# Optimization experiments

Measured on AMD Instinct MI355X. Metric: run time of the kernel, lower is better.

The kernel has to match this reference:

```python
import jax, jax.numpy as jnp
import numpy as np

CH = 64          # channels
OC = 64          # out_channels
B, H, W = 8, 128, 128
NCA_C = CH + OC  # 128, NCA state channels
K = 3            # kernel_size
DILS = (1, 2, 4, 8)
HID = 64         # NCA update hidden
EPS = 1e-5


def setup_inputs() -> dict:
    key = jax.random.key(0)
    ks = jax.random.split(key, 16)
    def n(k, shape, s=0.02):
        return jax.random.normal(k, shape, jnp.float32) * s
    return {
        "x": jax.random.normal(ks[0], (B, H, W, CH), jnp.float32),
        "c": jax.random.normal(ks[1], (B, OC), jnp.float32),
        # Attention params
        "Wq": n(ks[2], (CH, OC)), "bq": jnp.zeros((OC,), jnp.float32),
        "Wk": n(ks[3], (OC, OC)), "bk": jnp.zeros((OC,), jnp.float32),
        "Wv": n(ks[4], (OC, OC)), "bv": jnp.zeros((OC,), jnp.float32),
        "Wo": n(ks[5], (OC, OC)), "bo": jnp.zeros((OC,), jnp.float32),
        "ln_g": jnp.ones((OC,), jnp.float32), "ln_b": jnp.zeros((OC,), jnp.float32),
        # NCA depthwise perception kernels, one per dilation: [4, NCA_C, 1, K, K]
        "pk": n(ks[6], (len(DILS), NCA_C, 1, K, K), 0.1),
        # NCA update MLP
        "W1": n(ks[7], ((1 + len(DILS)) * NCA_C, HID)), "b1": jnp.zeros((HID,), jnp.float32),
        "W2": n(ks[8], (HID, CH)), "b2": jnp.zeros((CH,), jnp.float32),
    }


def _layernorm(z, g, b):
    m = jnp.mean(z, axis=-1, keepdims=True)
    v = jnp.var(z, axis=-1, keepdims=True)
    return (z - m) / jnp.sqrt(v + EPS) * g + b


def _forward(x, c, Wq, bq, Wk, bk, Wv, bv, Wo, bo, ln_g, ln_b, pk, W1, b1, W2, b2):
    b_, h_, w_, _ = x.shape
    # ---- Attention(x, c): single-key softmax pooling over H*W ----
    q = x.reshape(b_, h_ * w_, CH) @ Wq + bq              # [B, HW, OC]
    k = c @ Wk + bk                                        # [B, OC]
    v = c @ Wv + bv                                        # [B, OC]
    scores = jnp.einsum('bno,bo->bn', q, k) * (OC ** -0.5)  # [B, HW]
    attn = jax.nn.softmax(scores, axis=1)                  # softmax over spatial dim
    attended = jnp.einsum('bn,bo->bo', attn, v)            # weighted pool (weights sum to 1)
    a = _layernorm(attended @ Wo + bo + c, ln_g, ln_b)     # out_proj + residual + LN
    c2 = c + a                                             # outer residual in NCAAttention

    # ---- concat broadcast context -> NCA state [B,H,W,NCA_C] ----
    c_exp = jnp.broadcast_to(c2[:, None, None, :], (b_, h_, w_, OC))
    xc = jnp.concatenate([x, c_exp], axis=-1)

    # ---- NCA perception: depthwise dilated convs (SAME padding) ----
    xp = jnp.transpose(xc, (0, 3, 1, 2))                   # NCHW
    feats = [xc]
    for i, d in enumerate(DILS):
        pad = d * (K // 2)
        p = jax.lax.conv_general_dilated(
            xp, pk[i], window_strides=(1, 1),
            padding=[(pad, pad), (pad, pad)], rhs_dilation=(d, d),
            dimension_numbers=('NCHW', 'OIHW', 'NCHW'),
            feature_group_count=NCA_C)
        feats.append(jnp.transpose(p, (0, 2, 3, 1)))
    upd_in = jnp.concatenate(feats, axis=-1)               # [B,H,W,5*NCA_C]

    # ---- NCA update MLP: Linear -> (Dropout=id) -> GELU -> Linear ----
    hidden = jax.nn.gelu(upd_in @ W1 + b1, approximate=False)
    y = hidden @ W2 + b2                                   # [B,H,W,CH]
    # NCA.out_channels (64) != NCA.channels (128) -> no residual add
    return y, c2


def reference(x, c, Wq, bq, Wk, bk, Wv, bv, Wo, bo, ln_g, ln_b, pk, W1, b1, W2, b2):
    return _forward(x, c, Wq, bq, Wk, bk, Wv, bv, Wo, bo, ln_g, ln_b, pk, W1, b1, W2, b2)
```

## Files before the change

kernel.cpp:

```cpp
#include <hip/hip_runtime.h>
#include <hip/hip_bf16.h>
#include <math.h>


typedef float  f32x4  __attribute__((ext_vector_type(4)));
typedef float  f32x16 __attribute__((ext_vector_type(16)));
typedef short  s16x8  __attribute__((ext_vector_type(8)));
typedef int    i32x4  __attribute__((ext_vector_type(4)));
typedef int    i32x8  __attribute__((ext_vector_type(8)));

static __device__ __forceinline__ unsigned short f2bf(float f) {
    __hip_bfloat16 h = __float2bfloat16(f);
    unsigned short u; __builtin_memcpy(&u, &h, 2); return u;
}
static __device__ __forceinline__ unsigned pk4fp8(float f0, float f1, float f2, float f3) {
    int v = 0;
    v = __builtin_amdgcn_cvt_pk_fp8_f32(f0, f1, v, false);
    v = __builtin_amdgcn_cvt_pk_fp8_f32(f2, f3, v, true);
    return (unsigned)v;
}

#define XROWB  9216
#define XBATCH 1327104
#define USCALE 256.0f

__global__ void prep2(const float* __restrict__ x,  const float* __restrict__ pk,
                      const float* __restrict__ W1, const float* __restrict__ W2,
                      const float* __restrict__ b1,
                      const float* __restrict__ c,
                      const float* __restrict__ Wv, const float* __restrict__ bv,
                      const float* __restrict__ Wo, const float* __restrict__ bo,
                      const float* __restrict__ lng, const float* __restrict__ lnb,
                      unsigned char* __restrict__ xp, unsigned char* __restrict__ Uf,
                      unsigned short* __restrict__ W2s,
                      float* __restrict__ V, float* __restrict__ hcp,
                      float* __restrict__ outc2)
{
    const int blk = blockIdx.x, tid = threadIdx.x;
    __shared__ float sc[512], sv[512], c2s[512];

    if (blk >= 667) {
        sc[tid] = c[tid]; sc[tid + 256] = c[tid + 256];
        __syncthreads();
        #pragma unroll
        for (int half = 0; half < 2; ++half) {
            int it = tid + half*256;
            int bb = it >> 6, j = it & 63;
            float v = bv[j];
            for (int i = 0; i < 64; ++i) v += sc[bb*64 + i]*Wv[i*64 + j];
            sv[it] = v;
        }
        __syncthreads();
        #pragma unroll
        for (int half = 0; half < 2; ++half) {
            int it = tid + half*256;
            int bb = it >> 6, j = it & 63;
            float t = bo[j] + sc[it];
            for (int i = 0; i < 64; ++i) t += sv[bb*64 + i]*Wo[i*64 + j];
            float s = t;
            for (int o = 32; o > 0; o >>= 1) s += __shfl_xor(s, o);
            float m = s * (1.f/64.f);
            float dq = (t - m)*(t - m);
            for (int o = 32; o > 0; o >>= 1) dq += __shfl_xor(dq, o);
            float a = (t - m) / sqrtf(dq*(1.f/64.f) + 1e-5f) * lng[j] + lnb[j];
            c2s[it] = sc[it] + a;
        }
        __syncthreads();
    }

    if (blk < 512) {
        const int ci = tid & 15;
        #pragma unroll 4
        for (int it = 0; it < 16; ++it) {
            int px = blk*256 + it*16 + (tid >> 4);
            int xc = px & 127, y = (px >> 7) & 127, b = px >> 14;
            float4 f = *(const float4*)(x + (size_t)px*64 + ci*4);
            unsigned P = pk4fp8(f.x, f.y, f.z, f.w);
            *(unsigned*)(xp + (size_t)b*XBATCH + (size_t)(y+8)*XROWB
                            + (size_t)(xc+8)*64 + ci*4) = P;
        }
    } else if (blk < 648) {
        int idx = (blk - 512)*256 + tid;
        int b = idx / 4352, r = idx - b*4352;
        int yy, xx;
        if (r < 2304) { int ry = r / 144; xx = r - ry*144; yy = (ry < 8) ? ry : 128 + ry; }
        else { int r2 = r - 2304; yy = 8 + (r2 >> 4); int xi = r2 & 15; xx = (xi < 8) ? xi : 128 + xi; }
        unsigned char* d = xp + (size_t)b*XBATCH + (size_t)yy*XROWB + (size_t)xx*64;
        uint4 z = make_uint4(0,0,0,0);
        *(uint4*)(d) = z; *(uint4*)(d+16) = z; *(uint4*)(d+32) = z; *(uint4*)(d+48) = z;
    } else if (blk < 665) {
        int idx = (blk - 648)*256 + tid;
        if (idx < 4224) {
            int lane = idx & 63, nt = (idx >> 6) & 1, pos = idx >> 7;
            int n  = nt*32 + (lane & 31);
            int h  = lane >> 5;
            static constexpr int DI[33] = {3,3,3, 2,2,2, 1,1,1, 0,0,0, -1, 0,0, 1,1, 2,2, 3,3,
                                           0,0,0, 1,1,1, 2,2,2, 3,3,3};
            static constexpr int TT[33] = {0,1,2, 0,1,2, 0,1,2, 0,1,2, 4, 3,5, 3,5, 3,5, 3,5,
                                           6,7,8, 6,7,8, 6,7,8, 6,7,8};
            int di = DI[pos], t = TT[pos];
            float vv[32];
            #pragma unroll
            for (int j = 0; j < 32; ++j) {
                int ch = h*32 + j;
                float v;
                if (di < 0) {
                    v = W1[ch*64 + n];
                    for (int dd = 0; dd < 4; ++dd)
                        v += pk[(dd*128 + ch)*9 + 4] * W1[((1+dd)*128 + ch)*64 + n];
                } else {
                    v = pk[(di*128 + ch)*9 + t] * W1[((1+di)*128 + ch)*64 + n];
                }
                vv[j] = v * USCALE;
            }
            unsigned char* base = Uf + (size_t)pos*4096 + nt*2048 + lane*16;
            uint4 o0, o1;
            o0.x = pk4fp8(vv[0],  vv[1],  vv[2],  vv[3]);
            o0.y = pk4fp8(vv[4],  vv[5],  vv[6],  vv[7]);
            o0.z = pk4fp8(vv[8],  vv[9],  vv[10], vv[11]);
            o0.w = pk4fp8(vv[12], vv[13], vv[14], vv[15]);
            o1.x = pk4fp8(vv[16], vv[17], vv[18], vv[19]);
            o1.y = pk4fp8(vv[20], vv[21], vv[22], vv[23]);
            o1.z = pk4fp8(vv[24], vv[25], vv[26], vv[27]);
            o1.w = pk4fp8(vv[28], vv[29], vv[30], vv[31]);
            *(uint4*)(base)        = o0;
            *(uint4*)(base + 1024) = o1;
        }
    } else if (blk < 667) {
        int idx = (blk - 665)*256 + tid;
        int lane = idx & 63, nt = (idx >> 6) & 3, kc2 = (idx >> 8) & 1;
        int n  = nt*16 + (lane & 15);
        int k0 = kc2*32 + (lane >> 4)*8;
        unsigned short e[8];
        #pragma unroll
        for (int j = 0; j < 8; ++j) e[j] = f2bf(W2[(k0+j)*64 + n]);
        uint4 o;
        o.x = (unsigned)e[0] | ((unsigned)e[1] << 16);
        o.y = (unsigned)e[2] | ((unsigned)e[3] << 16);
        o.z = (unsigned)e[4] | ((unsigned)e[5] << 16);
        o.w = (unsigned)e[6] | ((unsigned)e[7] << 16);
        *(uint4*)(W2s + (size_t)idx*8) = o;
    } else if (blk < 739) {
        int idx = (blk - 667)*256 + tid;
        int n = idx & 63, q = idx >> 6;
        int p = q % 36, b = q / 36;
        int di = p/9, t = p%9;
        float s = 0.f;
        for (int j = 0; j < 64; ++j)
            s += c2s[b*64 + j] * pk[(di*128 + 64 + j)*9 + t] * W1[((1+di)*128 + 64 + j)*64 + n];
        V[(size_t)q*64 + n] = s;
    } else {
        for (int it = tid; it < 512; it += 256) {
            int b = it >> 6, n = it & 63;
            float s = b1[n];
            for (int j = 0; j < 64; ++j) s += c2s[b*64 + j]*W1[(64 + j)*64 + n];
            hcp[it] = s;
            outc2[it] = c2s[it];
        }
    }
}

#define HID_S 72

__global__ __launch_bounds__(512, 4) void nca_main(
    const unsigned char* __restrict__ xp,
    const unsigned char* __restrict__ U,
    const unsigned short* __restrict__ W2s,
    const float* __restrict__ V,
    const float* __restrict__ hcp,
    const float* __restrict__ b2,
    float* __restrict__ out)
{
    __shared__ __align__(16) unsigned char smem[65536];
    __shared__ float V_l[36*64];
    __shared__ float Cx_l[16*64];
    __shared__ float Cy_l[2*64];
    __shared__ float hc2_l[64];

    unsigned short* hid = (unsigned short*)smem;

    const int tid = threadIdx.x;
    const int blk = blockIdx.x;
    const int b  = blk & 7;
    const int y0 = (blk >> 3) * 2;

    #pragma unroll
    for (int s = 0; s < 4; ++s) {
        int off = tid*16 + s*8192;
        __builtin_amdgcn_global_load_lds(
            (const __attribute__((address_space(1))) unsigned int*)(U + off),
            (__attribute__((address_space(3))) unsigned int*)(smem + off),
            16, 0, 0);
    }

    {
        const float4* Vg = (const float4*)(V + (size_t)b*2304);
        for (int i = tid; i < 576; i += 512) ((float4*)V_l)[i] = Vg[i];
    }
    __syncthreads();
    for (int it = tid; it < 1024; it += 512) {
        int xi = it >> 6, n = it & 63;
        int xx = xi < 8 ? xi : 112 + xi;
        float s = 0.f;
        #pragma unroll
        for (int di = 0; di < 4; ++di) {
            int d = 1 << di;
            int dxo = (xx < d) ? 0 : ((xx >= 128 - d) ? 2 : -1);
            if (dxo >= 0) {
                s += V_l[(di*9 + 0*3 + dxo)*64 + n];
                s += V_l[(di*9 + 1*3 + dxo)*64 + n];
                s += V_l[(di*9 + 2*3 + dxo)*64 + n];
            }
        }
        Cx_l[it] = s;
    }
    if (tid < 128) {
        int r = tid >> 6, n = tid & 63;
        int yy = y0 + r;
        float s = 0.f;
        #pragma unroll
        for (int di = 0; di < 4; ++di) {
            int d = 1 << di;
            int dyo = (yy < d) ? 0 : ((yy >= 128 - d) ? 2 : -1);
            if (dyo >= 0) {
                s += V_l[(di*9 + dyo*3 + 0)*64 + n];
                s += V_l[(di*9 + dyo*3 + 1)*64 + n];
                s += V_l[(di*9 + dyo*3 + 2)*64 + n];
            }
        }
        Cy_l[tid] = s;
    } else if (tid < 192) {
        int n = tid - 128;
        float s = hcp[b*64 + n];
        for (int p = 0; p < 36; ++p) s += V_l[p*64 + n];
        hc2_l[n] = s;
    }
    __syncthreads();

    const int lane = tid & 63;
    const int w    = tid >> 6;
    const int rib  = w >> 2;
    const int y    = y0 + rib;
    const int xw   = (w & 3) * 32;
    const int ln15 = lane & 15;
    const int oct  = lane >> 4;
    const int l31  = lane & 31;
    const int kg   = lane >> 5;

    const unsigned char* abase = xp + (size_t)b*XBATCH + (size_t)(y + 8)*XROWB
                               + (size_t)(xw + l31 + 8)*64 + kg*32;

    f32x16 acc[2];
    #pragma unroll
    for (int nt = 0; nt < 2; ++nt)
        #pragma unroll
        for (int r = 0; r < 16; ++r) acc[nt][r] = 0.f;

    static constexpr int OFF[33] = {
        (-8*144-8)*64, (-8*144)*64, (-8*144+8)*64,
        (-4*144-4)*64, (-4*144)*64, (-4*144+4)*64,
        (-2*144-2)*64, (-2*144)*64, (-2*144+2)*64,
        (-1*144-1)*64, (-1*144)*64, (-1*144+1)*64,
        0,
        -64, 64, -128, 128, -256, 256, -512, 512,
        ( 1*144-1)*64, ( 1*144)*64, ( 1*144+1)*64,
        ( 2*144-2)*64, ( 2*144)*64, ( 2*144+2)*64,
        ( 4*144-4)*64, ( 4*144)*64, ( 4*144+4)*64,
        ( 8*144-8)*64, ( 8*144)*64, ( 8*144+8)*64
    };

    auto loadB = [&](int cofs, int p, i32x8* Bv) {
        const unsigned char* rp = smem + cofs + p*4096 + lane*16;
        #pragma unroll
        for (int nt = 0; nt < 2; ++nt) {
            i32x4 lo = *(const i32x4*)(rp + nt*2048);
            i32x4 hi = *(const i32x4*)(rp + nt*2048 + 1024);
            i32x8 v;
            v[0]=lo[0]; v[1]=lo[1]; v[2]=lo[2]; v[3]=lo[3];
            v[4]=hi[0]; v[5]=hi[1]; v[6]=hi[2]; v[7]=hi[3];
            Bv[nt] = v;
        }
    };

    i32x8 Areg[2];
    i32x8 Breg[2][2];
    Areg[0] = *(const i32x8*)(abase + OFF[0]);
    loadB(0, 0, Breg[0]);

    int cur = 0;
    #pragma unroll 1
    for (int kb = 0; kb < 4; ++kb) {
        {
            const int nbytes = (kb < 3) ? 32768 : 4096;
            const unsigned char* gsrc = U + (size_t)(kb + 1)*32768;
            unsigned char* ldst = smem + (cur ^ 1)*32768;
            for (int off = tid*16; off < nbytes; off += 8192)
                __builtin_amdgcn_global_load_lds(
                    (const __attribute__((address_space(1))) unsigned int*)(gsrc + off),
                    (__attribute__((address_space(3))) unsigned int*)(ldst + off),
                    16, 0, 0);
        }
        const int cofs = cur*32768;
        #pragma unroll
        for (int p = 0; p < 8; ++p) {
            const int pos = kb*8 + p;
            Areg[(p + 1) & 1] = *(const i32x8*)(abase + OFF[pos + 1]);
            if (p < 7) loadB(cofs, p + 1, Breg[(p + 1) & 1]);
            __builtin_amdgcn_s_setprio(1);
            acc[0] = __builtin_amdgcn_mfma_scale_f32_32x32x64_f8f6f4(
                Areg[p & 1], Breg[p & 1][0], acc[0], 0, 0, 0, 0x7F7F7F7F, 0, 0x7F7F7F7F);
            acc[1] = __builtin_amdgcn_mfma_scale_f32_32x32x64_f8f6f4(
                Areg[p & 1], Breg[p & 1][1], acc[1], 0, 0, 0, 0x7F7F7F7F, 0, 0x7F7F7F7F);
            __builtin_amdgcn_s_setprio(0);
        }
        __syncthreads();
        cur ^= 1;
        loadB(cur*32768, 0, Breg[0]);
    }
    __builtin_amdgcn_s_setprio(1);
    acc[0] = __builtin_amdgcn_mfma_scale_f32_32x32x64_f8f6f4(
        Areg[0], Breg[0][0], acc[0], 0, 0, 0, 0x7F7F7F7F, 0, 0x7F7F7F7F);
    acc[1] = __builtin_amdgcn_mfma_scale_f32_32x32x64_f8f6f4(
        Areg[0], Breg[0][1], acc[1], 0, 0, 0, 0x7F7F7F7F, 0, 0x7F7F7F7F);
    __builtin_amdgcn_s_setprio(0);
    __syncthreads();

    const bool yedge = (y < 8) || (y >= 120);
    #pragma unroll
    for (int nt = 0; nt < 2; ++nt) {
        const int n = nt*32 + l31;
        const float hcv = hc2_l[n];
        const float cyv = yedge ? Cy_l[rib*64 + n] : 0.f;
        #pragma unroll
        for (int reg = 0; reg < 16; ++reg) {
            int row = (reg & 3) + 8*(reg >> 2) + 4*kg;
            int x = xw + row;
            float h = acc[nt][reg]*(1.0f/USCALE) + hcv - cyv;
            if (x < 8 || x >= 120) {
                int xi = (x < 8) ? x : (x - 112);
                h -= Cx_l[xi*64 + n];
                if (yedge) {
                    #pragma unroll
                    for (int di = 0; di < 4; ++di) {
                        int d = 1 << di;
                        int dyo = (y < d) ? 0 : ((y >= 128 - d) ? 2 : -1);
                        int dxo = (x < d) ? 0 : ((x >= 128 - d) ? 2 : -1);
                        if (dyo >= 0 && dxo >= 0)
                            h += V_l[(di*9 + dyo*3 + dxo)*64 + n];
                    }
                }
            }
            float u = 0.7978845608028654f * (h + 0.044715f*h*h*h);
            float g = h / (1.f + __expf(-2.f*u));
            hid[(rib*128 + x)*HID_S + n] = f2bf(g);
        }
    }

    f32x4 acc2[2][4];
    #pragma unroll
    for (int mt = 0; mt < 2; ++mt)
        #pragma unroll
        for (int nt = 0; nt < 4; ++nt) {
            acc2[mt][nt][0] = 0.f; acc2[mt][nt][1] = 0.f;
            acc2[mt][nt][2] = 0.f; acc2[mt][nt][3] = 0.f;
        }
    #pragma unroll
    for (int kc2 = 0; kc2 < 2; ++kc2) {
        s16x8 a2[2];
        #pragma unroll
        for (int mt = 0; mt < 2; ++mt)
            a2[mt] = *(const s16x8*)&hid[(rib*128 + xw + mt*16 + ln15)*HID_S + kc2*32 + oct*8];
        #pragma unroll
        for (int nt = 0; nt < 4; ++nt) {
            s16x8 bfr = *(const s16x8*)(W2s + ((size_t)(kc2*4 + nt)*64 + lane)*8);
            #pragma unroll
            for (int mt = 0; mt < 2; ++mt)
                acc2[mt][nt] = __builtin_amdgcn_mfma_f32_16x16x32_bf16(a2[mt], bfr, acc2[mt][nt], 0, 0, 0);
        }
    }

    float* ob = out + ((size_t)(b*128 + y))*128*64;
    #pragma unroll
    for (int nt = 0; nt < 4; ++nt) {
        const float b2v = b2[nt*16 + ln15];
        #pragma unroll
        for (int mt = 0; mt < 2; ++mt) {
            #pragma unroll
            for (int r = 0; r < 4; ++r) {
                int x = xw + mt*16 + oct*4 + r;
                ob[(size_t)x*64 + nt*16 + ln15] = acc2[mt][nt][r] + b2v;
            }
        }
    }
}

extern "C" void kernel_launch(void* const* d_in, const int* in_sizes, int n_in,
                              void* d_out, int out_size, void* d_ws, size_t ws_size,
                              hipStream_t stream) {
    const float* x   = (const float*)d_in[0];
    const float* c   = (const float*)d_in[1];
    const float* Wv  = (const float*)d_in[6];
    const float* bv  = (const float*)d_in[7];
    const float* Wo  = (const float*)d_in[8];
    const float* bo  = (const float*)d_in[9];
    const float* lng = (const float*)d_in[10];
    const float* lnb = (const float*)d_in[11];
    const float* pk  = (const float*)d_in[12];
    const float* W1  = (const float*)d_in[13];
    const float* b1  = (const float*)d_in[14];
    const float* W2  = (const float*)d_in[15];
    const float* b2  = (const float*)d_in[16];
    float* out = (float*)d_out;

    char* w = (char*)d_ws;
    unsigned char*  xpb = (unsigned char*)(w);
    unsigned char*  Uf  = (unsigned char*)(w + 10616832);
    unsigned short* W2s = (unsigned short*)(w + 10752000);
    float*          V   = (float*)         (w + 10760192);
    float*          hcp = (float*)         (w + 10833920);

    prep2<<<740, 256, 0, stream>>>(x, pk, W1, W2, b1, c, Wv, bv, Wo, bo, lng, lnb,
                                   xpb, Uf, W2s, V, hcp, out + 8388608);
    nca_main<<<512, 512, 0, stream>>>(xpb, Uf, W2s, V, hcp, b2, out);
}
```

Measured before the change: 150.3 us.

## Process four rows per block so each B tile feeds two row strips

Each nca_main block now covers four image rows instead of two. Every wave accumulates two row strips against the same LDS-staged fp8 weight fragments, which halves the grid and halves the number of times the U weight matrix is streamed into LDS per output. The A-operand prefetch is deepened to a 4-slot ring, three positions ahead. The epilogue processes the two strips one after another, using a per-wave hidden buffer. In exchange, registers per thread roughly double (launch bounds drop to 2 blocks per CU) and the grid shrinks to 256 blocks, which reduces occupancy and parallelism.

```diff
diff --git a/kernel.cpp b/kernel.cpp
--- a/kernel.cpp
+++ b/kernel.cpp
@@ -162,7 +162,7 @@
 
 #define HID_S 72
 
-__global__ __launch_bounds__(512, 4) void nca_main(
+__global__ __launch_bounds__(512, 2) void nca_main(
     const unsigned char* __restrict__ xp,
     const unsigned char* __restrict__ U,
     const unsigned short* __restrict__ W2s,
@@ -174,7 +174,7 @@
     __shared__ __align__(16) unsigned char smem[65536];
     __shared__ float V_l[36*64];
     __shared__ float Cx_l[16*64];
-    __shared__ float Cy_l[2*64];
+    __shared__ float Cy_l[4*64];
     __shared__ float hc2_l[64];
 
     unsigned short* hid = (unsigned short*)smem;
@@ -182,7 +182,7 @@
     const int tid = threadIdx.x;
     const int blk = blockIdx.x;
     const int b  = blk & 7;
-    const int y0 = (blk >> 3) * 2;
+    const int y0 = (blk >> 3) * 4;
 
     #pragma unroll
     for (int s = 0; s < 4; ++s) {
@@ -214,7 +214,7 @@
         }
         Cx_l[it] = s;
     }
-    if (tid < 128) {
+    if (tid < 256) {
         int r = tid >> 6, n = tid & 63;
         int yy = y0 + r;
         float s = 0.f;
@@ -229,8 +229,8 @@
             }
         }
         Cy_l[tid] = s;
-    } else if (tid < 192) {
-        int n = tid - 128;
+    } else if (tid < 320) {
+        int n = tid - 256;
         float s = hcp[b*64 + n];
         for (int p = 0; p < 36; ++p) s += V_l[p*64 + n];
         hc2_l[n] = s;
@@ -239,22 +239,27 @@
 
     const int lane = tid & 63;
     const int w    = tid >> 6;
-    const int rib  = w >> 2;
-    const int y    = y0 + rib;
     const int xw   = (w & 3) * 32;
     const int ln15 = lane & 15;
     const int oct  = lane >> 4;
     const int l31  = lane & 31;
     const int kg   = lane >> 5;
 
-    const unsigned char* abase = xp + (size_t)b*XBATCH + (size_t)(y + 8)*XROWB
-                               + (size_t)(xw + l31 + 8)*64 + kg*32;
-
-    f32x16 acc[2];
+    const unsigned char* abase[2];
     #pragma unroll
-    for (int nt = 0; nt < 2; ++nt)
-        #pragma unroll
-        for (int r = 0; r < 16; ++r) acc[nt][r] = 0.f;
+    for (int s = 0; s < 2; ++s) {
+        int row = (w >> 2) + s*2;
+        abase[s] = xp + (size_t)b*XBATCH + (size_t)(y0 + row + 8)*XROWB
+                 + (size_t)(xw + l31 + 8)*64 + kg*32;
+    }
+
+    f32x16 acc[2][2];
+    #pragma unroll
+    for (int s = 0; s < 2; ++s)
+        #pragma unroll
+        for (int nt = 0; nt < 2; ++nt)
+            #pragma unroll
+            for (int r = 0; r < 16; ++r) acc[s][nt][r] = 0.f;
 
     static constexpr int OFF[33] = {
         (-8*144-8)*64, (-8*144)*64, (-8*144+8)*64,
@@ -282,9 +287,14 @@
         }
     };
 
-    i32x8 Areg[2];
+    i32x8 Areg[2][4];
     i32x8 Breg[2][2];
-    Areg[0] = *(const i32x8*)(abase + OFF[0]);
+    #pragma unroll
+    for (int s = 0; s < 2; ++s) {
+        Areg[s][0] = *(const i32x8*)(abase[s] + OFF[0]);
+        Areg[s][1] = *(const i32x8*)(abase[s] + OFF[1]);
+        Areg[s][2] = *(const i32x8*)(abase[s] + OFF[2]);
+    }
     loadB(0, 0, Breg[0]);
 
     int cur = 0;
@@ -304,13 +314,19 @@
         #pragma unroll
         for (int p = 0; p < 8; ++p) {
             const int pos = kb*8 + p;
-            Areg[(p + 1) & 1] = *(const i32x8*)(abase + OFF[pos + 1]);
+            const int pf  = (pos + 3 > 32) ? 32 : (pos + 3);
+            #pragma unroll
+            for (int s = 0; s < 2; ++s)
+                Areg[s][(pos + 3) & 3] = *(const i32x8*)(abase[s] + OFF[pf]);
             if (p < 7) loadB(cofs, p + 1, Breg[(p + 1) & 1]);
             __builtin_amdgcn_s_setprio(1);
-            acc[0] = __builtin_amdgcn_mfma_scale_f32_32x32x64_f8f6f4(
-                Areg[p & 1], Breg[p & 1][0], acc[0], 0, 0, 0, 0x7F7F7F7F, 0, 0x7F7F7F7F);
-            acc[1] = __builtin_amdgcn_mfma_scale_f32_32x32x64_f8f6f4(
-                Areg[p & 1], Breg[p & 1][1], acc[1], 0, 0, 0, 0x7F7F7F7F, 0, 0x7F7F7F7F);
+            #pragma unroll
+            for (int s = 0; s < 2; ++s) {
+                acc[s][0] = __builtin_amdgcn_mfma_scale_f32_32x32x64_f8f6f4(
+                    Areg[s][pos & 3], Breg[p & 1][0], acc[s][0], 0, 0, 0, 0x7F7F7F7F, 0, 0x7F7F7F7F);
+                acc[s][1] = __builtin_amdgcn_mfma_scale_f32_32x32x64_f8f6f4(
+                    Areg[s][pos & 3], Breg[p & 1][1], acc[s][1], 0, 0, 0, 0x7F7F7F7F, 0, 0x7F7F7F7F);
+            }
             __builtin_amdgcn_s_setprio(0);
         }
         __syncthreads();
@@ -318,77 +334,86 @@
         loadB(cur*32768, 0, Breg[0]);
     }
     __builtin_amdgcn_s_setprio(1);
-    acc[0] = __builtin_amdgcn_mfma_scale_f32_32x32x64_f8f6f4(
-        Areg[0], Breg[0][0], acc[0], 0, 0, 0, 0x7F7F7F7F, 0, 0x7F7F7F7F);
-    acc[1] = __builtin_amdgcn_mfma_scale_f32_32x32x64_f8f6f4(
-        Areg[0], Breg[0][1], acc[1], 0, 0, 0, 0x7F7F7F7F, 0, 0x7F7F7F7F);
+    #pragma unroll
+    for (int s = 0; s < 2; ++s) {
+        acc[s][0] = __builtin_amdgcn_mfma_scale_f32_32x32x64_f8f6f4(
+            Areg[s][0], Breg[0][0], acc[s][0], 0, 0, 0, 0x7F7F7F7F, 0, 0x7F7F7F7F);
+        acc[s][1] = __builtin_amdgcn_mfma_scale_f32_32x32x64_f8f6f4(
+            Areg[s][0], Breg[0][1], acc[s][1], 0, 0, 0, 0x7F7F7F7F, 0, 0x7F7F7F7F);
+    }
     __builtin_amdgcn_s_setprio(0);
     __syncthreads();
 
-    const bool yedge = (y < 8) || (y >= 120);
-    #pragma unroll
-    for (int nt = 0; nt < 2; ++nt) {
-        const int n = nt*32 + l31;
-        const float hcv = hc2_l[n];
-        const float cyv = yedge ? Cy_l[rib*64 + n] : 0.f;
-        #pragma unroll
-        for (int reg = 0; reg < 16; ++reg) {
-            int row = (reg & 3) + 8*(reg >> 2) + 4*kg;
-            int x = xw + row;
-            float h = acc[nt][reg]*(1.0f/USCALE) + hcv - cyv;
-            if (x < 8 || x >= 120) {
-                int xi = (x < 8) ? x : (x - 112);
-                h -= Cx_l[xi*64 + n];
-                if (yedge) {
-                    #pragma unroll
-                    for (int di = 0; di < 4; ++di) {
-                        int d = 1 << di;
-                        int dyo = (y < d) ? 0 : ((y >= 128 - d) ? 2 : -1);
-                        int dxo = (x < d) ? 0 : ((x >= 128 - d) ? 2 : -1);
-                        if (dyo >= 0 && dxo >= 0)
-                            h += V_l[(di*9 + dyo*3 + dxo)*64 + n];
+    unsigned short* hw = hid + w*32*HID_S;
+    #pragma unroll 1
+    for (int s = 0; s < 2; ++s) {
+        const int row = (w >> 2) + s*2;
+        const int y   = y0 + row;
+        const bool yedge = (y < 8) || (y >= 120);
+        #pragma unroll
+        for (int nt = 0; nt < 2; ++nt) {
+            const int n = nt*32 + l31;
+            const float hcv = hc2_l[n];
+            const float cyv = yedge ? Cy_l[row*64 + n] : 0.f;
+            #pragma unroll
+            for (int reg = 0; reg < 16; ++reg) {
+                int xr = (reg & 3) + 8*(reg >> 2) + 4*kg;
+                int x = xw + xr;
+                float h = acc[s][nt][reg]*(1.0f/USCALE) + hcv - cyv;
+                if (x < 8 || x >= 120) {
+                    int xi = (x < 8) ? x : (x - 112);
+                    h -= Cx_l[xi*64 + n];
+                    if (yedge) {
+                        #pragma unroll
+                        for (int di = 0; di < 4; ++di) {
+                            int d = 1 << di;
+                            int dyo = (y < d) ? 0 : ((y >= 128 - d) ? 2 : -1);
+                            int dxo = (x < d) ? 0 : ((x >= 128 - d) ? 2 : -1);
+                            if (dyo >= 0 && dxo >= 0)
+                                h += V_l[(di*9 + dyo*3 + dxo)*64 + n];
+                        }
                     }
                 }
-            }
-            float u = 0.7978845608028654f * (h + 0.044715f*h*h*h);
-            float g = h / (1.f + __expf(-2.f*u));
-            hid[(rib*128 + x)*HID_S + n] = f2bf(g);
-        }
-    }
-
-    f32x4 acc2[2][4];
-    #pragma unroll
-    for (int mt = 0; mt < 2; ++mt)
+                float u = 0.7978845608028654f * (h + 0.044715f*h*h*h);
+                float g = h / (1.f + __expf(-2.f*u));
+                hw[xr*HID_S + n] = f2bf(g);
+            }
+        }
+
+        f32x4 acc2[2][4];
+        #pragma unroll
+        for (int mt = 0; mt < 2; ++mt)
+            #pragma unroll
+            for (int nt = 0; nt < 4; ++nt) {
+                acc2[mt][nt][0] = 0.f; acc2[mt][nt][1] = 0.f;
+                acc2[mt][nt][2] = 0.f; acc2[mt][nt][3] = 0.f;
+            }
+        #pragma unroll
+        for (int kc2 = 0; kc2 < 2; ++kc2) {
+            s16x8 a2[2];
+            #pragma unroll
+            for (int mt = 0; mt < 2; ++mt)
+                a2[mt] = *(const s16x8*)&hw[(mt*16 + ln15)*HID_S + kc2*32 + oct*8];
+            #pragma unroll
+            for (int nt = 0; nt < 4; ++nt) {
+                s16x8 bfr = *(const s16x8*)(W2s + ((size_t)(kc2*4 + nt)*64 + lane)*8);
+                #pragma unroll
+                for (int mt = 0; mt < 2; ++mt)
+                    acc2[mt][nt] = __builtin_amdgcn_mfma_f32_16x16x32_bf16(a2[mt], bfr, acc2[mt][nt], 0, 0, 0);
+            }
+        }
+
+        float* ob = out + ((size_t)(b*128 + y))*128*64;
         #pragma unroll
         for (int nt = 0; nt < 4; ++nt) {
-            acc2[mt][nt][0] = 0.f; acc2[mt][nt][1] = 0.f;
-            acc2[mt][nt][2] = 0.f; acc2[mt][nt][3] = 0.f;
-        }
-    #pragma unroll
-    for (int kc2 = 0; kc2 < 2; ++kc2) {
-        s16x8 a2[2];
-        #pragma unroll
-        for (int mt = 0; mt < 2; ++mt)
-            a2[mt] = *(const s16x8*)&hid[(rib*128 + xw + mt*16 + ln15)*HID_S + kc2*32 + oct*8];
-        #pragma unroll
-        for (int nt = 0; nt < 4; ++nt) {
-            s16x8 bfr = *(const s16x8*)(W2s + ((size_t)(kc2*4 + nt)*64 + lane)*8);
-            #pragma unroll
-            for (int mt = 0; mt < 2; ++mt)
-                acc2[mt][nt] = __builtin_amdgcn_mfma_f32_16x16x32_bf16(a2[mt], bfr, acc2[mt][nt], 0, 0, 0);
-        }
-    }
-
-    float* ob = out + ((size_t)(b*128 + y))*128*64;
-    #pragma unroll
-    for (int nt = 0; nt < 4; ++nt) {
-        const float b2v = b2[nt*16 + ln15];
-        #pragma unroll
-        for (int mt = 0; mt < 2; ++mt) {
-            #pragma unroll
-            for (int r = 0; r < 4; ++r) {
-                int x = xw + mt*16 + oct*4 + r;
-                ob[(size_t)x*64 + nt*16 + ln15] = acc2[mt][nt][r] + b2v;
+            const float b2v = b2[nt*16 + ln15];
+            #pragma unroll
+            for (int mt = 0; mt < 2; ++mt) {
+                #pragma unroll
+                for (int r = 0; r < 4; ++r) {
+                    int x = xw + mt*16 + oct*4 + r;
+                    ob[(size_t)x*64 + nt*16 + ln15] = acc2[mt][nt][r] + b2v;
+                }
             }
         }
     }
@@ -421,5 +446,5 @@
 
     prep2<<<740, 256, 0, stream>>>(x, pk, W1, W2, b1, c, Wv, bv, Wo, bo, lng, lnb,
                                    xpb, Uf, W2s, V, hcp, out + 8388608);
-    nca_main<<<512, 512, 0, stream>>>(xpb, Uf, W2s, V, hcp, b2, out);
+    nca_main<<<256, 512, 0, stream>>>(xpb, Uf, W2s, V, hcp, b2, out);
 }
```

Result: slower. 187.4 us (+24.7%).
